# Performance work log

Measured on AMD Instinct MI355X. Metric: run time of the kernel, lower is better.

Reference implementation:

```python
import jax, jax.numpy as jnp
import numpy as np

B, T, D, N = 32, 512, 128, 1024
NOISE = 0.001
SPECTRAL_RADIUS = 1.0


def setup_inputs() -> dict:
    key = jax.random.key(0)
    ks = jax.random.split(key, 7)
    x = jax.random.normal(ks[0], (B, T, D), dtype=jnp.float32)
    # w_input = uniform[0,1)*2 - 1
    w_input = jax.random.uniform(ks[1], (D, N), dtype=jnp.float32) * 2 - 1
    # w_reservoir = uniform[0,1) - 0.5, then rescaled to target spectral radius
    w_res = jax.random.uniform(ks[2], (N, N), dtype=jnp.float32) - 0.5
    radius = float(np.max(np.abs(np.linalg.eigvals(np.asarray(w_res, dtype=np.float32)))))
    w_res = w_res * jnp.float32(SPECTRAL_RADIUS / radius)
    w_scale_input = jax.random.uniform(ks[3], (), dtype=jnp.float32)
    states0 = jax.random.normal(ks[4], (B, N), dtype=jnp.float32)
    step0 = jax.random.normal(ks[5], (B, N), dtype=jnp.float32)
    random_noise = jax.random.normal(ks[6], (B, N), dtype=jnp.float32)
    return {
        "x": x,
        "w_input": w_input,
        "w_reservoir": w_res,
        "w_scale_input": w_scale_input,
        "states0": states0,
        "step0": step0,
        "random_noise": random_noise,
    }


def reference(x, w_input, w_reservoir, w_scale_input, states0, step0, random_noise):
    # Precompute scaled input projections for steps 1..T-1 (parallel matmul)
    xin = jnp.einsum("btd,dn->btn", x[:, 1:, :], w_input) * w_scale_input  # [B,T-1,N]

    def step(states, xt):
        pre = states @ w_reservoir + xt
        post = jnp.tanh(pre) + NOISE * random_noise
        return post, post

    _, ys = jax.lax.scan(step, states0, jnp.swapaxes(xin, 0, 1))  # ys: [T-1,B,N]
    out = jnp.concatenate([step0[:, None, :], jnp.swapaxes(ys, 0, 1)], axis=1)  # [B,T,N]
    return out[..., None]  # [B,T,N,1]
```

## Files before the change

### kernel.cpp

```cpp
#include <hip/hip_runtime.h>
#include <hip/hip_bf16.h>
#include <math.h>

#define B_  32
#define T_  512
#define D_  128
#define N_  1024
#define NOISE_ 0.001f

#define NBLK 64
#define CPB  16

typedef __attribute__((ext_vector_type(8))) short  bf16x8;
typedef __attribute__((ext_vector_type(4))) float  f32x4;

static __device__ __forceinline__ unsigned short f2bf_rn(float f) {
    unsigned int u = __builtin_bit_cast(unsigned int, f);
    unsigned int r = (u + 0x7FFFu + ((u >> 16) & 1u)) >> 16;
    return (unsigned short)r;
}
static __device__ __forceinline__ float bf2f(unsigned short h) {
    return __builtin_bit_cast(float, (unsigned int)h << 16);
}

__global__ __launch_bounds__(256) void xin_gemm(
    const float* __restrict__ x, const float* __restrict__ w_in,
    const float* __restrict__ scale_p, float* __restrict__ out) {
  __shared__ float As[64 * 132];
  __shared__ float Bs[128 * 68];
  const int tid = threadIdx.x;
  const int bm = blockIdx.x;
  const int bn = blockIdx.y;

  {
    const f32x4* xg = (const f32x4*)(x + (size_t)bm * 64 * 128);
#pragma unroll
    for (int i = 0; i < 8; ++i) {
      int idx = tid + i * 256;
      int r = idx >> 5, c4 = idx & 31;
      f32x4 v = xg[idx];
      float* dst = &As[r * 132 + c4 * 4];
      dst[0] = v.x; dst[1] = v.y; dst[2] = v.z; dst[3] = v.w;
    }
  }
  {
#pragma unroll
    for (int i = 0; i < 8; ++i) {
      int idx = tid + i * 256;
      int r = idx >> 4, c4 = idx & 15;
      f32x4 v = *(const f32x4*)(w_in + (size_t)r * N_ + bn * 64 + c4 * 4);
      float* dst = &Bs[r * 68 + c4 * 4];
      dst[0] = v.x; dst[1] = v.y; dst[2] = v.z; dst[3] = v.w;
    }
  }
  __syncthreads();

  const int tx = tid & 15, ty = tid >> 4;
  float acc[4][4] = {};
  for (int k = 0; k < 128; ++k) {
    float a0 = As[(ty * 4 + 0) * 132 + k];
    float a1 = As[(ty * 4 + 1) * 132 + k];
    float a2 = As[(ty * 4 + 2) * 132 + k];
    float a3 = As[(ty * 4 + 3) * 132 + k];
    f32x4 bv = *(const f32x4*)&Bs[k * 68 + tx * 4];
#pragma unroll
    for (int j = 0; j < 4; ++j) {
      acc[0][j] += a0 * bv[j];
      acc[1][j] += a1 * bv[j];
      acc[2][j] += a2 * bv[j];
      acc[3][j] += a3 * bv[j];
    }
  }
  const float s = scale_p[0];
#pragma unroll
  for (int i = 0; i < 4; ++i) {
    int row = bm * 64 + ty * 4 + i;
    if ((row & 511) == 0) continue;
    f32x4 o;
    o.x = acc[i][0] * s; o.y = acc[i][1] * s;
    o.z = acc[i][2] * s; o.w = acc[i][3] * s;
    *(f32x4*)(out + (size_t)row * N_ + bn * 64 + tx * 4) = o;
  }
}

__global__ __launch_bounds__(256) void init_k(
    const float* __restrict__ states0, const float* __restrict__ step0,
    float* __restrict__ out, unsigned short* __restrict__ st_hi,
    unsigned short* __restrict__ st_lo, int* __restrict__ flags) {
  int i = blockIdx.x * 256 + threadIdx.x;
  if (i < B_ * N_) {
    int b = i >> 10, n = i & 1023;
    out[((size_t)b * T_ + 0) * N_ + n] = step0[i];
    float sv = states0[i];
    unsigned short h = f2bf_rn(sv);
    st_hi[i] = h;
    st_lo[i] = f2bf_rn(sv - bf2f(h));
  }
  if (i < 1024) flags[i] = 0;
}

__global__ __launch_bounds__(256, 1) void esn_rec(
    const float* __restrict__ w_res, const float* __restrict__ rn,
    float* __restrict__ out, unsigned short* __restrict__ st_hi,
    unsigned short* __restrict__ st_lo, int* flags) {
  __shared__ bf16x8 wHi8[CPB * 129];
  __shared__ bf16x8 wLo8[CPB * 129];
  __shared__ float  pLDS[4 * 32 * 17];

  const int tid = threadIdx.x;
  const int blk = blockIdx.x;

  {
    unsigned short* wH = (unsigned short*)wHi8;
    unsigned short* wL = (unsigned short*)wLo8;
    for (int i = tid; i < CPB * 1024; i += 256) {
      int c = i & 15, k = i >> 4;
      float wv = w_res[(size_t)k * N_ + blk * CPB + c];
      unsigned short h = f2bf_rn(wv);
      wH[c * 1032 + k] = h;
      wL[c * 1032 + k] = f2bf_rn(wv - bf2f(h));
    }
  }
  __syncthreads();

  const int lane = tid & 63, wave = tid >> 6;
  const int quad = lane >> 4, lm = lane & 15;

  const int rm = tid >> 3;
  const int cp = (tid & 7) * 2;
  const int colg = blk * CPB + cp;
  float2 nz = *(const float2*)&rn[(size_t)rm * N_ + colg];
  nz.x *= NOISE_; nz.y *= NOISE_;

  const int vo0 = lm * 2048 + wave * 512 + quad * 16;
  const int vo1 = vo0 + 16 * 2048;

  for (int t = 1; t < T_; ++t) {
    const int pc = (t - 1) & 1, ncur = t & 1;

    size_t o0 = ((size_t)rm * T_ + t) * N_ + colg;
    float2 xv = *(const float2*)&out[o0];

    {
      const int need = t - 1;
      const int fidx = (wave * 16 + (lane & 15)) * 16;
      while (true) {
        int f = __hip_atomic_load(&flags[fidx], __ATOMIC_RELAXED,
                                  __HIP_MEMORY_SCOPE_SYSTEM);
        if (__all(f >= need)) break;
      }
    }

    const char* baseH = (const char*)(st_hi + pc * (B_ * N_));
    const char* baseL = (const char*)(st_lo + pc * (B_ * N_));
    bf16x8 AH0[8], AH1[8], AL0[8], AL1[8];
#pragma unroll
    for (int kk = 0; kk < 8; ++kk) {
      int oa = vo0 + kk * 64, ob = vo1 + kk * 64;
      asm volatile("global_load_dwordx4 %0, %1, %2 sc0 sc1"
                   : "=v"(AH0[kk]) : "v"(oa), "s"(baseH) : "memory");
      asm volatile("global_load_dwordx4 %0, %1, %2 sc0 sc1"
                   : "=v"(AH1[kk]) : "v"(ob), "s"(baseH) : "memory");
      asm volatile("global_load_dwordx4 %0, %1, %2 sc0 sc1"
                   : "=v"(AL0[kk]) : "v"(oa), "s"(baseL) : "memory");
      asm volatile("global_load_dwordx4 %0, %1, %2 sc0 sc1"
                   : "=v"(AL1[kk]) : "v"(ob), "s"(baseL) : "memory");
    }
    asm volatile("s_waitcnt vmcnt(0)" ::: "memory");

    f32x4 acc0 = {0.f, 0.f, 0.f, 0.f};
    f32x4 acc1 = {0.f, 0.f, 0.f, 0.f};
#pragma unroll
    for (int kk = 0; kk < 8; ++kk) {
      const int k8 = wave * 32 + kk * 4 + quad;
      bf16x8 bh = wHi8[lm * 129 + k8];
      bf16x8 bl = wLo8[lm * 129 + k8];
      acc0 = __builtin_amdgcn_mfma_f32_16x16x32_bf16(AH0[kk], bh, acc0, 0, 0, 0);
      acc1 = __builtin_amdgcn_mfma_f32_16x16x32_bf16(AH1[kk], bh, acc1, 0, 0, 0);
      acc0 = __builtin_amdgcn_mfma_f32_16x16x32_bf16(AL0[kk], bh, acc0, 0, 0, 0);
      acc1 = __builtin_amdgcn_mfma_f32_16x16x32_bf16(AL1[kk], bh, acc1, 0, 0, 0);
      acc0 = __builtin_amdgcn_mfma_f32_16x16x32_bf16(AH0[kk], bl, acc0, 0, 0, 0);
      acc1 = __builtin_amdgcn_mfma_f32_16x16x32_bf16(AH1[kk], bl, acc1, 0, 0, 0);
    }

#pragma unroll
    for (int r = 0; r < 4; ++r) {
      pLDS[wave * 544 + (quad * 4 + r) * 17 + lm]      = acc0[r];
      pLDS[wave * 544 + (quad * 4 + r + 16) * 17 + lm] = acc1[r];
    }
    __syncthreads();

    float sa = pLDS[0 * 544 + rm * 17 + cp] + pLDS[1 * 544 + rm * 17 + cp]
             + pLDS[2 * 544 + rm * 17 + cp] + pLDS[3 * 544 + rm * 17 + cp];
    float sb = pLDS[0 * 544 + rm * 17 + cp + 1] + pLDS[1 * 544 + rm * 17 + cp + 1]
             + pLDS[2 * 544 + rm * 17 + cp + 1] + pLDS[3 * 544 + rm * 17 + cp + 1];
    float v0 = tanhf(sa + xv.x) + nz.x;
    float v1 = tanhf(sb + xv.y) + nz.y;
    float2 ov; ov.x = v0; ov.y = v1;
    *(float2*)&out[o0] = ov;

    unsigned short h0 = f2bf_rn(v0), h1 = f2bf_rn(v1);
    unsigned short l0 = f2bf_rn(v0 - bf2f(h0)), l1 = f2bf_rn(v1 - bf2f(h1));
    unsigned int hpack = (unsigned int)h0 | ((unsigned int)h1 << 16);
    unsigned int lpack = (unsigned int)l0 | ((unsigned int)l1 << 16);
    unsigned int* dh = (unsigned int*)(st_hi + ncur * (B_ * N_) + (size_t)rm * N_ + colg);
    unsigned int* dl = (unsigned int*)(st_lo + ncur * (B_ * N_) + (size_t)rm * N_ + colg);
    __hip_atomic_store(dh, hpack, __ATOMIC_RELAXED, __HIP_MEMORY_SCOPE_SYSTEM);
    __hip_atomic_store(dl, lpack, __ATOMIC_RELAXED, __HIP_MEMORY_SCOPE_SYSTEM);

    asm volatile("s_waitcnt vmcnt(0)" ::: "memory");
    __syncthreads();
    if (tid == 0) {
      __hip_atomic_store(&flags[blk * 16], t, __ATOMIC_RELAXED,
                         __HIP_MEMORY_SCOPE_SYSTEM);
    }
  }
}

extern "C" void kernel_launch(void* const* d_in, const int* in_sizes, int n_in,
                              void* d_out, int out_size, void* d_ws, size_t ws_size,
                              hipStream_t stream) {
  const float* x       = (const float*)d_in[0];
  const float* w_in    = (const float*)d_in[1];
  const float* w_res   = (const float*)d_in[2];
  const float* wscale  = (const float*)d_in[3];
  const float* states0 = (const float*)d_in[4];
  const float* step0   = (const float*)d_in[5];
  const float* rnoise  = (const float*)d_in[6];
  float* out = (float*)d_out;

  char* ws = (char*)d_ws;
  unsigned short* st_hi = (unsigned short*)ws;
  unsigned short* st_lo = (unsigned short*)(ws + 131072);
  int* flags            = (int*)(ws + 262144);

  xin_gemm<<<dim3(256, 16), 256, 0, stream>>>(x, w_in, wscale, out);
  init_k<<<128, 256, 0, stream>>>(states0, step0, out, st_hi, st_lo, flags);
  esn_rec<<<NBLK, 256, 0, stream>>>(w_res, rnoise, out, st_hi, st_lo, flags);
}
```

Before: 3.118 ms.

## Hold reservoir weights in registers, halve workgroups, overlap state loads with MFMA

The persistent recurrence kernel now runs on 32 workgroups of 32 columns each instead of 64 of 16. The hi/lo bf16 weight slices live in VGPRs rather than LDS, which removes the per-step LDS weight reads. Each step issues its state loads and then starts MFMAs on the first half once those loads land, overlapping the rest of the load latency with compute. Fewer workgroups means fewer flags to poll per step, at the cost of more per-workgroup MFMA work and high register pressure.

```diff
diff --git a/kernel.cpp b/kernel.cpp
--- a/kernel.cpp
+++ b/kernel.cpp
@@ -8,8 +8,8 @@
 #define N_  1024
 #define NOISE_ 0.001f
 
-#define NBLK 64
-#define CPB  16
+#define NWORK 32
+#define CPB   32
 
 typedef __attribute__((ext_vector_type(8))) short  bf16x8;
 typedef __attribute__((ext_vector_type(4))) float  f32x4;
@@ -103,47 +103,60 @@
     const float* __restrict__ w_res, const float* __restrict__ rn,
     float* __restrict__ out, unsigned short* __restrict__ st_hi,
     unsigned short* __restrict__ st_lo, int* flags) {
-  __shared__ bf16x8 wHi8[CPB * 129];
-  __shared__ bf16x8 wLo8[CPB * 129];
-  __shared__ float  pLDS[4 * 32 * 17];
+  __shared__ float pLDS[4 * 32 * 33];
 
   const int tid = threadIdx.x;
   const int blk = blockIdx.x;
 
-  {
-    unsigned short* wH = (unsigned short*)wHi8;
-    unsigned short* wL = (unsigned short*)wLo8;
-    for (int i = tid; i < CPB * 1024; i += 256) {
-      int c = i & 15, k = i >> 4;
-      float wv = w_res[(size_t)k * N_ + blk * CPB + c];
-      unsigned short h = f2bf_rn(wv);
-      wH[c * 1032 + k] = h;
-      wL[c * 1032 + k] = f2bf_rn(wv - bf2f(h));
-    }
-  }
-  __syncthreads();
-
   const int lane = tid & 63, wave = tid >> 6;
   const int quad = lane >> 4, lm = lane & 15;
 
+  bf16x8 BH[8][2], BL[8][2];
+#pragma unroll
+  for (int kk = 0; kk < 8; ++kk) {
+#pragma unroll
+    for (int ct = 0; ct < 2; ++ct) {
+      const float* wp = w_res + (size_t)(wave * 256 + kk * 32 + quad * 8) * N_
+                              + blk * CPB + ct * 16 + lm;
+      bf16x8 hv, lv;
+#pragma unroll
+      for (int j = 0; j < 8; ++j) {
+        float wv = wp[(size_t)j * N_];
+        unsigned short h = f2bf_rn(wv);
+        hv[j] = (short)h;
+        lv[j] = (short)f2bf_rn(wv - bf2f(h));
+      }
+      BH[kk][ct] = hv;
+      BL[kk][ct] = lv;
+    }
+  }
+
   const int rm = tid >> 3;
-  const int cp = (tid & 7) * 2;
-  const int colg = blk * CPB + cp;
-  float2 nz = *(const float2*)&rn[(size_t)rm * N_ + colg];
-  nz.x *= NOISE_; nz.y *= NOISE_;
+  const int cg = (tid & 7) * 4;
+  const int colg = blk * CPB + cg;
+  float4 nz = *(const float4*)&rn[(size_t)rm * N_ + colg];
+  nz.x *= NOISE_; nz.y *= NOISE_; nz.z *= NOISE_; nz.w *= NOISE_;
 
   const int vo0 = lm * 2048 + wave * 512 + quad * 16;
   const int vo1 = vo0 + 16 * 2048;
+  const int fidx = (wave * 8 + (lane & 7)) * 16;
+
+  __syncthreads();
 
   for (int t = 1; t < T_; ++t) {
     const int pc = (t - 1) & 1, ncur = t & 1;
 
     size_t o0 = ((size_t)rm * T_ + t) * N_ + colg;
-    float2 xv = *(const float2*)&out[o0];
+    f32x4 xv;
+    {
+      int loff = (int)(o0 * 4);
+      const char* ob = (const char*)out;
+      asm volatile("global_load_dwordx4 %0, %1, %2"
+                   : "=v"(xv) : "v"(loff), "s"(ob) : "memory");
+    }
 
     {
       const int need = t - 1;
-      const int fidx = (wave * 16 + (lane & 15)) * 16;
       while (true) {
         int f = __hip_atomic_load(&flags[fidx], __ATOMIC_RELAXED,
                                   __HIP_MEMORY_SCOPE_SYSTEM);
@@ -166,47 +179,85 @@
       asm volatile("global_load_dwordx4 %0, %1, %2 sc0 sc1"
                    : "=v"(AL1[kk]) : "v"(ob), "s"(baseL) : "memory");
     }
+
+    f32x4 acc00 = {0.f, 0.f, 0.f, 0.f};
+    f32x4 acc01 = {0.f, 0.f, 0.f, 0.f};
+    f32x4 acc10 = {0.f, 0.f, 0.f, 0.f};
+    f32x4 acc11 = {0.f, 0.f, 0.f, 0.f};
+
+    asm volatile("s_waitcnt vmcnt(16)" ::: "memory");
+    __builtin_amdgcn_sched_barrier(0);
+#pragma unroll
+    for (int kk = 0; kk < 4; ++kk) {
+      acc00 = __builtin_amdgcn_mfma_f32_16x16x32_bf16(AH0[kk], BH[kk][0], acc00, 0, 0, 0);
+      acc01 = __builtin_amdgcn_mfma_f32_16x16x32_bf16(AH1[kk], BH[kk][0], acc01, 0, 0, 0);
+      acc10 = __builtin_amdgcn_mfma_f32_16x16x32_bf16(AH0[kk], BH[kk][1], acc10, 0, 0, 0);
+      acc11 = __builtin_amdgcn_mfma_f32_16x16x32_bf16(AH1[kk], BH[kk][1], acc11, 0, 0, 0);
+      acc00 = __builtin_amdgcn_mfma_f32_16x16x32_bf16(AL0[kk], BH[kk][0], acc00, 0, 0, 0);
+      acc01 = __builtin_amdgcn_mfma_f32_16x16x32_bf16(AL1[kk], BH[kk][0], acc01, 0, 0, 0);
+      acc10 = __builtin_amdgcn_mfma_f32_16x16x32_bf16(AL0[kk], BH[kk][1], acc10, 0, 0, 0);
+      acc11 = __builtin_amdgcn_mfma_f32_16x16x32_bf16(AL1[kk], BH[kk][1], acc11, 0, 0, 0);
+      acc00 = __builtin_amdgcn_mfma_f32_16x16x32_bf16(AH0[kk], BL[kk][0], acc00, 0, 0, 0);
+      acc01 = __builtin_amdgcn_mfma_f32_16x16x32_bf16(AH1[kk], BL[kk][0], acc01, 0, 0, 0);
+      acc10 = __builtin_amdgcn_mfma_f32_16x16x32_bf16(AH0[kk], BL[kk][1], acc10, 0, 0, 0);
+      acc11 = __builtin_amdgcn_mfma_f32_16x16x32_bf16(AH1[kk], BL[kk][1], acc11, 0, 0, 0);
+    }
     asm volatile("s_waitcnt vmcnt(0)" ::: "memory");
-
-    f32x4 acc0 = {0.f, 0.f, 0.f, 0.f};
-    f32x4 acc1 = {0.f, 0.f, 0.f, 0.f};
-#pragma unroll
-    for (int kk = 0; kk < 8; ++kk) {
-      const int k8 = wave * 32 + kk * 4 + quad;
-      bf16x8 bh = wHi8[lm * 129 + k8];
-      bf16x8 bl = wLo8[lm * 129 + k8];
-      acc0 = __builtin_amdgcn_mfma_f32_16x16x32_bf16(AH0[kk], bh, acc0, 0, 0, 0);
-      acc1 = __builtin_amdgcn_mfma_f32_16x16x32_bf16(AH1[kk], bh, acc1, 0, 0, 0);
-      acc0 = __builtin_amdgcn_mfma_f32_16x16x32_bf16(AL0[kk], bh, acc0, 0, 0, 0);
-      acc1 = __builtin_amdgcn_mfma_f32_16x16x32_bf16(AL1[kk], bh, acc1, 0, 0, 0);
-      acc0 = __builtin_amdgcn_mfma_f32_16x16x32_bf16(AH0[kk], bl, acc0, 0, 0, 0);
-      acc1 = __builtin_amdgcn_mfma_f32_16x16x32_bf16(AH1[kk], bl, acc1, 0, 0, 0);
+    __builtin_amdgcn_sched_barrier(0);
+#pragma unroll
+    for (int kk = 4; kk < 8; ++kk) {
+      acc00 = __builtin_amdgcn_mfma_f32_16x16x32_bf16(AH0[kk], BH[kk][0], acc00, 0, 0, 0);
+      acc01 = __builtin_amdgcn_mfma_f32_16x16x32_bf16(AH1[kk], BH[kk][0], acc01, 0, 0, 0);
+      acc10 = __builtin_amdgcn_mfma_f32_16x16x32_bf16(AH0[kk], BH[kk][1], acc10, 0, 0, 0);
+      acc11 = __builtin_amdgcn_mfma_f32_16x16x32_bf16(AH1[kk], BH[kk][1], acc11, 0, 0, 0);
+      acc00 = __builtin_amdgcn_mfma_f32_16x16x32_bf16(AL0[kk], BH[kk][0], acc00, 0, 0, 0);
+      acc01 = __builtin_amdgcn_mfma_f32_16x16x32_bf16(AL1[kk], BH[kk][0], acc01, 0, 0, 0);
+      acc10 = __builtin_amdgcn_mfma_f32_16x16x32_bf16(AL0[kk], BH[kk][1], acc10, 0, 0, 0);
+      acc11 = __builtin_amdgcn_mfma_f32_16x16x32_bf16(AL1[kk], BH[kk][1], acc11, 0, 0, 0);
+      acc00 = __builtin_amdgcn_mfma_f32_16x16x32_bf16(AH0[kk], BL[kk][0], acc00, 0, 0, 0);
+      acc01 = __builtin_amdgcn_mfma_f32_16x16x32_bf16(AH1[kk], BL[kk][0], acc01, 0, 0, 0);
+      acc10 = __builtin_amdgcn_mfma_f32_16x16x32_bf16(AH0[kk], BL[kk][1], acc10, 0, 0, 0);
+      acc11 = __builtin_amdgcn_mfma_f32_16x16x32_bf16(AH1[kk], BL[kk][1], acc11, 0, 0, 0);
     }
 
 #pragma unroll
     for (int r = 0; r < 4; ++r) {
-      pLDS[wave * 544 + (quad * 4 + r) * 17 + lm]      = acc0[r];
-      pLDS[wave * 544 + (quad * 4 + r + 16) * 17 + lm] = acc1[r];
+      pLDS[wave * 1056 + (quad * 4 + r) * 33 + lm]           = acc00[r];
+      pLDS[wave * 1056 + (quad * 4 + r + 16) * 33 + lm]      = acc01[r];
+      pLDS[wave * 1056 + (quad * 4 + r) * 33 + 16 + lm]      = acc10[r];
+      pLDS[wave * 1056 + (quad * 4 + r + 16) * 33 + 16 + lm] = acc11[r];
     }
     __syncthreads();
 
-    float sa = pLDS[0 * 544 + rm * 17 + cp] + pLDS[1 * 544 + rm * 17 + cp]
-             + pLDS[2 * 544 + rm * 17 + cp] + pLDS[3 * 544 + rm * 17 + cp];
-    float sb = pLDS[0 * 544 + rm * 17 + cp + 1] + pLDS[1 * 544 + rm * 17 + cp + 1]
-             + pLDS[2 * 544 + rm * 17 + cp + 1] + pLDS[3 * 544 + rm * 17 + cp + 1];
-    float v0 = tanhf(sa + xv.x) + nz.x;
-    float v1 = tanhf(sb + xv.y) + nz.y;
-    float2 ov; ov.x = v0; ov.y = v1;
-    *(float2*)&out[o0] = ov;
+    float s0 = 0.f, s1 = 0.f, s2 = 0.f, s3 = 0.f;
+#pragma unroll
+    for (int w = 0; w < 4; ++w) {
+      const float* p = &pLDS[w * 1056 + rm * 33 + cg];
+      s0 += p[0]; s1 += p[1]; s2 += p[2]; s3 += p[3];
+    }
+    float v0 = tanhf(s0 + xv[0]) + nz.x;
+    float v1 = tanhf(s1 + xv[1]) + nz.y;
+    float v2 = tanhf(s2 + xv[2]) + nz.z;
+    float v3 = tanhf(s3 + xv[3]) + nz.w;
+    float4 ov; ov.x = v0; ov.y = v1; ov.z = v2; ov.w = v3;
+    *(float4*)&out[o0] = ov;
 
     unsigned short h0 = f2bf_rn(v0), h1 = f2bf_rn(v1);
+    unsigned short h2 = f2bf_rn(v2), h3 = f2bf_rn(v3);
     unsigned short l0 = f2bf_rn(v0 - bf2f(h0)), l1 = f2bf_rn(v1 - bf2f(h1));
-    unsigned int hpack = (unsigned int)h0 | ((unsigned int)h1 << 16);
-    unsigned int lpack = (unsigned int)l0 | ((unsigned int)l1 << 16);
-    unsigned int* dh = (unsigned int*)(st_hi + ncur * (B_ * N_) + (size_t)rm * N_ + colg);
-    unsigned int* dl = (unsigned int*)(st_lo + ncur * (B_ * N_) + (size_t)rm * N_ + colg);
-    __hip_atomic_store(dh, hpack, __ATOMIC_RELAXED, __HIP_MEMORY_SCOPE_SYSTEM);
-    __hip_atomic_store(dl, lpack, __ATOMIC_RELAXED, __HIP_MEMORY_SCOPE_SYSTEM);
+    unsigned short l2 = f2bf_rn(v2 - bf2f(h2)), l3 = f2bf_rn(v3 - bf2f(h3));
+    unsigned long long hp =
+        (unsigned long long)((unsigned int)h0 | ((unsigned int)h1 << 16)) |
+        ((unsigned long long)((unsigned int)h2 | ((unsigned int)h3 << 16)) << 32);
+    unsigned long long lp =
+        (unsigned long long)((unsigned int)l0 | ((unsigned int)l1 << 16)) |
+        ((unsigned long long)((unsigned int)l2 | ((unsigned int)l3 << 16)) << 32);
+    unsigned long long* dh =
+        (unsigned long long*)(st_hi + ncur * (B_ * N_) + (size_t)rm * N_ + colg);
+    unsigned long long* dl =
+        (unsigned long long*)(st_lo + ncur * (B_ * N_) + (size_t)rm * N_ + colg);
+    __hip_atomic_store(dh, hp, __ATOMIC_RELAXED, __HIP_MEMORY_SCOPE_SYSTEM);
+    __hip_atomic_store(dl, lp, __ATOMIC_RELAXED, __HIP_MEMORY_SCOPE_SYSTEM);
 
     asm volatile("s_waitcnt vmcnt(0)" ::: "memory");
     __syncthreads();
@@ -236,5 +287,5 @@
 
   xin_gemm<<<dim3(256, 16), 256, 0, stream>>>(x, w_in, wscale, out);
   init_k<<<128, 256, 0, stream>>>(states0, step0, out, st_hi, st_lo, flags);
-  esn_rec<<<NBLK, 256, 0, stream>>>(w_res, rnoise, out, st_hi, st_lo, flags);
-}
+  esn_rec<<<NWORK, 256, 0, stream>>>(w_res, rnoise, out, st_hi, st_lo, flags);
+}
```

Result: slower. 3.352 ms (+7.5%).

## Hold recurrent weights in registers and use per-wave flags with pipelined polling

Applied to the files above, without the earlier changes.

The recurrence kernel now keeps its bf16 hi/lo slices of the reservoir weights in VGPRs instead of LDS, removing the per-step LDS weight reads. Each wave publishes its own progress flag, so the end-of-step block barrier goes away. Flag polling uses two overlapping vector loads, and the MFMA chain starts on the first half of the state loads while the second half is still in flight. It also launches 192 extra spinner blocks that run dummy FMAs and loads until the recurrence finishes, apparently to keep the GPU busy or its clocks up. That costs power and risks deadlock if the worker blocks are not all resident together.

```diff
diff --git a/kernel.cpp b/kernel.cpp
--- a/kernel.cpp
+++ b/kernel.cpp
@@ -8,11 +8,14 @@
 #define N_  1024
 #define NOISE_ 0.001f
 
-#define NBLK 64
-#define CPB  16
+#define NWORK 64
+#define CPB   16
+#define GRID_REC 256
 
 typedef __attribute__((ext_vector_type(8))) short  bf16x8;
 typedef __attribute__((ext_vector_type(4))) float  f32x4;
+typedef __attribute__((ext_vector_type(2))) float  f32x2;
+typedef __attribute__((ext_vector_type(4))) int    i32x4;
 
 static __device__ __forceinline__ unsigned short f2bf_rn(float f) {
     unsigned int u = __builtin_bit_cast(unsigned int, f);
@@ -22,6 +25,7 @@
 static __device__ __forceinline__ float bf2f(unsigned short h) {
     return __builtin_bit_cast(float, (unsigned int)h << 16);
 }
+static __device__ __forceinline__ int imin(int a, int b) { return a < b ? a : b; }
 
 __global__ __launch_bounds__(256) void xin_gemm(
     const float* __restrict__ x, const float* __restrict__ w_in,
@@ -103,28 +107,54 @@
     const float* __restrict__ w_res, const float* __restrict__ rn,
     float* __restrict__ out, unsigned short* __restrict__ st_hi,
     unsigned short* __restrict__ st_lo, int* flags) {
-  __shared__ bf16x8 wHi8[CPB * 129];
-  __shared__ bf16x8 wLo8[CPB * 129];
-  __shared__ float  pLDS[4 * 32 * 17];
+  __shared__ float pLDS[4 * 32 * 17];
 
   const int tid = threadIdx.x;
-  const int blk = blockIdx.x;
-
-  {
-    unsigned short* wH = (unsigned short*)wHi8;
-    unsigned short* wL = (unsigned short*)wLo8;
-    for (int i = tid; i < CPB * 1024; i += 256) {
-      int c = i & 15, k = i >> 4;
-      float wv = w_res[(size_t)k * N_ + blk * CPB + c];
-      unsigned short h = f2bf_rn(wv);
-      wH[c * 1032 + k] = h;
-      wL[c * 1032 + k] = f2bf_rn(wv - bf2f(h));
-    }
-  }
-  __syncthreads();
-
+  const int bx = blockIdx.x;
+
+  if (bx >= NWORK) {
+    float hx = (float)(tid + bx);
+    const char* wb = (const char*)w_res;
+    int it = 0;
+    while (true) {
+      i32x4 f;
+      asm volatile("global_load_dwordx4 %0, %1, %2 sc0 sc1\n\ts_waitcnt vmcnt(0)"
+                   : "=v"(f) : "v"(0), "s"(flags) : "memory");
+      if (imin(imin(f.x, f.y), imin(f.z, f.w)) >= T_ - 1) break;
+#pragma unroll 8
+      for (int u = 0; u < 1024; ++u)
+        hx = __builtin_fmaf(hx, 1.0000001f, 1.0e-7f);
+      f32x4 dummy;
+      int off = (it & 16383) * 256;
+      asm volatile("global_load_dwordx4 %0, %1, %2 sc0\n\ts_waitcnt vmcnt(0)"
+                   : "=v"(dummy) : "v"(off), "s"(wb) : "memory");
+      asm volatile("" :: "v"(dummy));
+      ++it;
+    }
+    asm volatile("" :: "v"(hx));
+    return;
+  }
+
+  const int blk = bx;
   const int lane = tid & 63, wave = tid >> 6;
   const int quad = lane >> 4, lm = lane & 15;
+
+  bf16x8 BH[8], BL[8];
+#pragma unroll
+  for (int kk = 0; kk < 8; ++kk) {
+    const float* wp = w_res + (size_t)(wave * 256 + kk * 32 + quad * 8) * N_
+                            + blk * CPB + lm;
+    bf16x8 hv, lv;
+#pragma unroll
+    for (int j = 0; j < 8; ++j) {
+      float wv = wp[(size_t)j * N_];
+      unsigned short h = f2bf_rn(wv);
+      hv[j] = (short)h;
+      lv[j] = (short)f2bf_rn(wv - bf2f(h));
+    }
+    BH[kk] = hv;
+    BL[kk] = lv;
+  }
 
   const int rm = tid >> 3;
   const int cp = (tid & 7) * 2;
@@ -134,21 +164,40 @@
 
   const int vo0 = lm * 2048 + wave * 512 + quad * 16;
   const int vo1 = vo0 + 16 * 2048;
+  const int fbyte = (wave * 16 + (lane & 15)) * 64;
 
   for (int t = 1; t < T_; ++t) {
     const int pc = (t - 1) & 1, ncur = t & 1;
 
     size_t o0 = ((size_t)rm * T_ + t) * N_ + colg;
-    float2 xv = *(const float2*)&out[o0];
+    f32x2 xv;
+    {
+      int loff = (int)(o0 * 4);
+      asm volatile("global_load_dwordx2 %0, %1, %2"
+                   : "=v"(xv) : "v"(loff), "s"((const char*)out) : "memory");
+    }
 
     {
       const int need = t - 1;
-      const int fidx = (wave * 16 + (lane & 15)) * 16;
+      i32x4 fA, fB;
+      asm volatile("global_load_dwordx4 %0, %1, %2 sc0 sc1"
+                   : "=v"(fA) : "v"(fbyte), "s"(flags) : "memory");
+      asm volatile("global_load_dwordx4 %0, %1, %2 sc0 sc1"
+                   : "=v"(fB) : "v"(fbyte), "s"(flags) : "memory");
       while (true) {
-        int f = __hip_atomic_load(&flags[fidx], __ATOMIC_RELAXED,
-                                  __HIP_MEMORY_SCOPE_SYSTEM);
-        if (__all(f >= need)) break;
+        asm volatile("s_waitcnt vmcnt(1)" ::: "memory");
+        __builtin_amdgcn_sched_barrier(0);
+        if (__all(imin(imin(fA.x, fA.y), imin(fA.z, fA.w)) >= need)) break;
+        asm volatile("global_load_dwordx4 %0, %1, %2 sc0 sc1"
+                     : "=v"(fA) : "v"(fbyte), "s"(flags) : "memory");
+        asm volatile("s_waitcnt vmcnt(1)" ::: "memory");
+        __builtin_amdgcn_sched_barrier(0);
+        if (__all(imin(imin(fB.x, fB.y), imin(fB.z, fB.w)) >= need)) break;
+        asm volatile("global_load_dwordx4 %0, %1, %2 sc0 sc1"
+                     : "=v"(fB) : "v"(fbyte), "s"(flags) : "memory");
       }
+      asm volatile("s_waitcnt vmcnt(0)" ::: "memory");
+      __builtin_amdgcn_sched_barrier(0);
     }
 
     const char* baseH = (const char*)(st_hi + pc * (B_ * N_));
@@ -166,21 +215,31 @@
       asm volatile("global_load_dwordx4 %0, %1, %2 sc0 sc1"
                    : "=v"(AL1[kk]) : "v"(ob), "s"(baseL) : "memory");
     }
-    asm volatile("s_waitcnt vmcnt(0)" ::: "memory");
 
     f32x4 acc0 = {0.f, 0.f, 0.f, 0.f};
     f32x4 acc1 = {0.f, 0.f, 0.f, 0.f};
-#pragma unroll
-    for (int kk = 0; kk < 8; ++kk) {
-      const int k8 = wave * 32 + kk * 4 + quad;
-      bf16x8 bh = wHi8[lm * 129 + k8];
-      bf16x8 bl = wLo8[lm * 129 + k8];
-      acc0 = __builtin_amdgcn_mfma_f32_16x16x32_bf16(AH0[kk], bh, acc0, 0, 0, 0);
-      acc1 = __builtin_amdgcn_mfma_f32_16x16x32_bf16(AH1[kk], bh, acc1, 0, 0, 0);
-      acc0 = __builtin_amdgcn_mfma_f32_16x16x32_bf16(AL0[kk], bh, acc0, 0, 0, 0);
-      acc1 = __builtin_amdgcn_mfma_f32_16x16x32_bf16(AL1[kk], bh, acc1, 0, 0, 0);
-      acc0 = __builtin_amdgcn_mfma_f32_16x16x32_bf16(AH0[kk], bl, acc0, 0, 0, 0);
-      acc1 = __builtin_amdgcn_mfma_f32_16x16x32_bf16(AH1[kk], bl, acc1, 0, 0, 0);
+
+    asm volatile("s_waitcnt vmcnt(16)" ::: "memory");
+    __builtin_amdgcn_sched_barrier(0);
+#pragma unroll
+    for (int kk = 0; kk < 4; ++kk) {
+      acc0 = __builtin_amdgcn_mfma_f32_16x16x32_bf16(AH0[kk], BH[kk], acc0, 0, 0, 0);
+      acc1 = __builtin_amdgcn_mfma_f32_16x16x32_bf16(AH1[kk], BH[kk], acc1, 0, 0, 0);
+      acc0 = __builtin_amdgcn_mfma_f32_16x16x32_bf16(AL0[kk], BH[kk], acc0, 0, 0, 0);
+      acc1 = __builtin_amdgcn_mfma_f32_16x16x32_bf16(AL1[kk], BH[kk], acc1, 0, 0, 0);
+      acc0 = __builtin_amdgcn_mfma_f32_16x16x32_bf16(AH0[kk], BL[kk], acc0, 0, 0, 0);
+      acc1 = __builtin_amdgcn_mfma_f32_16x16x32_bf16(AH1[kk], BL[kk], acc1, 0, 0, 0);
+    }
+    asm volatile("s_waitcnt vmcnt(0)" ::: "memory");
+    __builtin_amdgcn_sched_barrier(0);
+#pragma unroll
+    for (int kk = 4; kk < 8; ++kk) {
+      acc0 = __builtin_amdgcn_mfma_f32_16x16x32_bf16(AH0[kk], BH[kk], acc0, 0, 0, 0);
+      acc1 = __builtin_amdgcn_mfma_f32_16x16x32_bf16(AH1[kk], BH[kk], acc1, 0, 0, 0);
+      acc0 = __builtin_amdgcn_mfma_f32_16x16x32_bf16(AL0[kk], BH[kk], acc0, 0, 0, 0);
+      acc1 = __builtin_amdgcn_mfma_f32_16x16x32_bf16(AL1[kk], BH[kk], acc1, 0, 0, 0);
+      acc0 = __builtin_amdgcn_mfma_f32_16x16x32_bf16(AH0[kk], BL[kk], acc0, 0, 0, 0);
+      acc1 = __builtin_amdgcn_mfma_f32_16x16x32_bf16(AH1[kk], BL[kk], acc1, 0, 0, 0);
     }
 
 #pragma unroll
@@ -194,8 +253,10 @@
              + pLDS[2 * 544 + rm * 17 + cp] + pLDS[3 * 544 + rm * 17 + cp];
     float sb = pLDS[0 * 544 + rm * 17 + cp + 1] + pLDS[1 * 544 + rm * 17 + cp + 1]
              + pLDS[2 * 544 + rm * 17 + cp + 1] + pLDS[3 * 544 + rm * 17 + cp + 1];
-    float v0 = tanhf(sa + xv.x) + nz.x;
-    float v1 = tanhf(sb + xv.y) + nz.y;
+    __syncthreads();
+
+    float v0 = tanhf(sa + xv[0]) + nz.x;
+    float v1 = tanhf(sb + xv[1]) + nz.y;
     float2 ov; ov.x = v0; ov.y = v1;
     *(float2*)&out[o0] = ov;
 
@@ -209,10 +270,9 @@
     __hip_atomic_store(dl, lpack, __ATOMIC_RELAXED, __HIP_MEMORY_SCOPE_SYSTEM);
 
     asm volatile("s_waitcnt vmcnt(0)" ::: "memory");
-    __syncthreads();
-    if (tid == 0) {
-      __hip_atomic_store(&flags[blk * 16], t, __ATOMIC_RELAXED,
-                         __HIP_MEMORY_SCOPE_SYSTEM);
+    if (lane == 0) {
+      asm volatile("global_store_dword %0, %1, %2 sc0 sc1"
+                   :: "v"((blk * 16 + wave) * 4), "v"(t), "s"(flags) : "memory");
     }
   }
 }
@@ -236,5 +296,5 @@
 
   xin_gemm<<<dim3(256, 16), 256, 0, stream>>>(x, w_in, wscale, out);
   init_k<<<128, 256, 0, stream>>>(states0, step0, out, st_hi, st_lo, flags);
-  esn_rec<<<NBLK, 256, 0, stream>>>(w_res, rnoise, out, st_hi, st_lo, flags);
-}
+  esn_rec<<<GRID_REC, 256, 0, stream>>>(w_res, rnoise, out, st_hi, st_lo, flags);
+}
```

New measurement: 3.367 ms. 8.0% more time.

## Embed parity tags in packed state words to replace flag-based inter-block sync

Applied to the files above, without the earlier changes.

Replaces the per-block flag barrier with step-parity bits stored in the low bit of the bf16 low-part words. The hi/lo state is interleaved into 16-byte packets written by one store, and consumers spin on a sentinel word and then validate every loaded packet's tag before using it. This removes the store-wait-syncthreads-flag round trip on each step. It also moves the reservoir weight slices from LDS into registers. The cost is a lost LSB in the lo part, extra tag checks and possible reload loops, and higher register pressure.

```diff
diff --git a/kernel.cpp b/kernel.cpp
--- a/kernel.cpp
+++ b/kernel.cpp
@@ -8,11 +8,13 @@
 #define N_  1024
 #define NOISE_ 0.001f
 
-#define NBLK 64
-#define CPB  16
+#define NWORK 64
+#define CPB   16
+#define SLOT_BYTES 131072
 
 typedef __attribute__((ext_vector_type(8))) short  bf16x8;
 typedef __attribute__((ext_vector_type(4))) float  f32x4;
+typedef __attribute__((ext_vector_type(4))) int    i32x4;
 
 static __device__ __forceinline__ unsigned short f2bf_rn(float f) {
     unsigned int u = __builtin_bit_cast(unsigned int, f);
@@ -85,46 +87,61 @@
 
 __global__ __launch_bounds__(256) void init_k(
     const float* __restrict__ states0, const float* __restrict__ step0,
-    float* __restrict__ out, unsigned short* __restrict__ st_hi,
-    unsigned short* __restrict__ st_lo, int* __restrict__ flags) {
+    float* __restrict__ out, char* __restrict__ stp) {
   int i = blockIdx.x * 256 + threadIdx.x;
   if (i < B_ * N_) {
     int b = i >> 10, n = i & 1023;
     out[((size_t)b * T_ + 0) * N_ + n] = step0[i];
-    float sv = states0[i];
-    unsigned short h = f2bf_rn(sv);
-    st_hi[i] = h;
-    st_lo[i] = f2bf_rn(sv - bf2f(h));
-  }
-  if (i < 1024) flags[i] = 0;
+  }
+  if (i < B_ * N_ / 4) {
+    int r = i >> 8, g = i & 255;
+    const float* sp = states0 + (size_t)r * N_ + g * 4;
+    unsigned int hw[4], lw[4];
+#pragma unroll
+    for (int j = 0; j < 4; ++j) {
+      float sv = sp[j];
+      unsigned short h = f2bf_rn(sv);
+      unsigned short l = f2bf_rn(sv - bf2f(h));
+      hw[j] = h;
+      lw[j] = (unsigned int)(l & 0xFFFEu);
+    }
+    i32x4 pkt;
+    pkt.x = (int)(hw[0] | (hw[1] << 16));
+    pkt.y = (int)(lw[0] | (lw[1] << 16));
+    pkt.z = (int)(hw[2] | (hw[3] << 16));
+    pkt.w = (int)(lw[2] | (lw[3] << 16));
+    *(i32x4*)(stp + (size_t)i * 16) = pkt;
+    i32x4 f1; f1.x = 0; f1.y = 0x00010000; f1.z = 0; f1.w = 0x00010000;
+    *(i32x4*)(stp + SLOT_BYTES + (size_t)i * 16) = f1;
+  }
 }
 
 __global__ __launch_bounds__(256, 1) void esn_rec(
     const float* __restrict__ w_res, const float* __restrict__ rn,
-    float* __restrict__ out, unsigned short* __restrict__ st_hi,
-    unsigned short* __restrict__ st_lo, int* flags) {
-  __shared__ bf16x8 wHi8[CPB * 129];
-  __shared__ bf16x8 wLo8[CPB * 129];
-  __shared__ float  pLDS[4 * 32 * 17];
+    float* __restrict__ out, char* stp) {
+  __shared__ float pLDS[4 * 32 * 17];
 
   const int tid = threadIdx.x;
   const int blk = blockIdx.x;
-
-  {
-    unsigned short* wH = (unsigned short*)wHi8;
-    unsigned short* wL = (unsigned short*)wLo8;
-    for (int i = tid; i < CPB * 1024; i += 256) {
-      int c = i & 15, k = i >> 4;
-      float wv = w_res[(size_t)k * N_ + blk * CPB + c];
-      unsigned short h = f2bf_rn(wv);
-      wH[c * 1032 + k] = h;
-      wL[c * 1032 + k] = f2bf_rn(wv - bf2f(h));
-    }
-  }
-  __syncthreads();
-
   const int lane = tid & 63, wave = tid >> 6;
   const int quad = lane >> 4, lm = lane & 15;
+
+  bf16x8 BH[8], BL[8];
+#pragma unroll
+  for (int kk = 0; kk < 8; ++kk) {
+    const float* wp = w_res + (size_t)(wave * 256 + kk * 32 + quad * 8) * N_
+                            + blk * CPB + lm;
+    bf16x8 hv, lv;
+#pragma unroll
+    for (int j = 0; j < 8; ++j) {
+      float wv = wp[(size_t)j * N_];
+      unsigned short h = f2bf_rn(wv);
+      hv[j] = (short)h;
+      lv[j] = (short)f2bf_rn(wv - bf2f(h));
+    }
+    BH[kk] = hv;
+    BL[kk] = lv;
+  }
 
   const int rm = tid >> 3;
   const int cp = (tid & 7) * 2;
@@ -132,55 +149,74 @@
   float2 nz = *(const float2*)&rn[(size_t)rm * N_ + colg];
   nz.x *= NOISE_; nz.y *= NOISE_;
 
-  const int vo0 = lm * 2048 + wave * 512 + quad * 16;
-  const int vo1 = vo0 + 16 * 2048;
+  const int vo0 = lm * 4096 + wave * 1024 + quad * 32;
+  const int vo1 = vo0 + 16 * 4096;
+  const int pp = wave * 16 + (lane & 15);
+  const int pbyte = ((lane >> 4) * 8 + 7) * 4096 + (pp * 4 + (lane >> 4)) * 16 + 4;
+  const int so = rm * 4096 + (blk * 4 + (cp >> 2)) * 16;
 
   for (int t = 1; t < T_; ++t) {
-    const int pc = (t - 1) & 1, ncur = t & 1;
+    const char* slotR = stp + ((t - 1) & 1) * SLOT_BYTES;
+    char* slotW = stp + (t & 1) * SLOT_BYTES;
+    const int want = ((t - 1) & 1) | ((((t - 1) >> 1) & 1) << 16);
 
     size_t o0 = ((size_t)rm * T_ + t) * N_ + colg;
     float2 xv = *(const float2*)&out[o0];
 
     {
-      const int need = t - 1;
-      const int fidx = (wave * 16 + (lane & 15)) * 16;
-      while (true) {
-        int f = __hip_atomic_load(&flags[fidx], __ATOMIC_RELAXED,
-                                  __HIP_MEMORY_SCOPE_SYSTEM);
-        if (__all(f >= need)) break;
+      int pr;
+      do {
+        asm volatile("global_load_dword %0, %1, %2 sc0 sc1\n\ts_waitcnt vmcnt(0)"
+                     : "=v"(pr) : "v"(pbyte), "s"(slotR) : "memory");
+      } while (!__all((pr & 0x00010001) == want));
+    }
+
+    i32x4 PA[8], PB[8], PC[8], PD[8];
+    while (true) {
+#pragma unroll
+      for (int kk = 0; kk < 8; ++kk) {
+        int oa = vo0 + kk * 128, ob = vo1 + kk * 128;
+        asm volatile("global_load_dwordx4 %0, %1, %2 sc0 sc1"
+                     : "=v"(PA[kk]) : "v"(oa), "s"(slotR) : "memory");
+        asm volatile("global_load_dwordx4 %0, %1, %2 sc0 sc1"
+                     : "=v"(PB[kk]) : "v"(oa + 16), "s"(slotR) : "memory");
+        asm volatile("global_load_dwordx4 %0, %1, %2 sc0 sc1"
+                     : "=v"(PC[kk]) : "v"(ob), "s"(slotR) : "memory");
+        asm volatile("global_load_dwordx4 %0, %1, %2 sc0 sc1"
+                     : "=v"(PD[kk]) : "v"(ob + 16), "s"(slotR) : "memory");
       }
-    }
-
-    const char* baseH = (const char*)(st_hi + pc * (B_ * N_));
-    const char* baseL = (const char*)(st_lo + pc * (B_ * N_));
-    bf16x8 AH0[8], AH1[8], AL0[8], AL1[8];
-#pragma unroll
-    for (int kk = 0; kk < 8; ++kk) {
-      int oa = vo0 + kk * 64, ob = vo1 + kk * 64;
-      asm volatile("global_load_dwordx4 %0, %1, %2 sc0 sc1"
-                   : "=v"(AH0[kk]) : "v"(oa), "s"(baseH) : "memory");
-      asm volatile("global_load_dwordx4 %0, %1, %2 sc0 sc1"
-                   : "=v"(AH1[kk]) : "v"(ob), "s"(baseH) : "memory");
-      asm volatile("global_load_dwordx4 %0, %1, %2 sc0 sc1"
-                   : "=v"(AL0[kk]) : "v"(oa), "s"(baseL) : "memory");
-      asm volatile("global_load_dwordx4 %0, %1, %2 sc0 sc1"
-                   : "=v"(AL1[kk]) : "v"(ob), "s"(baseL) : "memory");
-    }
-    asm volatile("s_waitcnt vmcnt(0)" ::: "memory");
+      asm volatile("s_waitcnt vmcnt(0)" ::: "memory");
+      __builtin_amdgcn_sched_barrier(0);
+      int err = 0;
+#pragma unroll
+      for (int kk = 0; kk < 8; ++kk) {
+        err |= (PA[kk].y ^ want) | (PA[kk].w ^ want);
+        err |= (PB[kk].y ^ want) | (PB[kk].w ^ want);
+        err |= (PC[kk].y ^ want) | (PC[kk].w ^ want);
+        err |= (PD[kk].y ^ want) | (PD[kk].w ^ want);
+      }
+      if (__all((err & 0x00010001) == 0)) break;
+    }
 
     f32x4 acc0 = {0.f, 0.f, 0.f, 0.f};
     f32x4 acc1 = {0.f, 0.f, 0.f, 0.f};
 #pragma unroll
     for (int kk = 0; kk < 8; ++kk) {
-      const int k8 = wave * 32 + kk * 4 + quad;
-      bf16x8 bh = wHi8[lm * 129 + k8];
-      bf16x8 bl = wLo8[lm * 129 + k8];
-      acc0 = __builtin_amdgcn_mfma_f32_16x16x32_bf16(AH0[kk], bh, acc0, 0, 0, 0);
-      acc1 = __builtin_amdgcn_mfma_f32_16x16x32_bf16(AH1[kk], bh, acc1, 0, 0, 0);
-      acc0 = __builtin_amdgcn_mfma_f32_16x16x32_bf16(AL0[kk], bh, acc0, 0, 0, 0);
-      acc1 = __builtin_amdgcn_mfma_f32_16x16x32_bf16(AL1[kk], bh, acc1, 0, 0, 0);
-      acc0 = __builtin_amdgcn_mfma_f32_16x16x32_bf16(AH0[kk], bl, acc0, 0, 0, 0);
-      acc1 = __builtin_amdgcn_mfma_f32_16x16x32_bf16(AH1[kk], bl, acc1, 0, 0, 0);
+      i32x4 h0i, l0i, h1i, l1i;
+      h0i.x = PA[kk].x; h0i.y = PA[kk].z; h0i.z = PB[kk].x; h0i.w = PB[kk].z;
+      l0i.x = PA[kk].y; l0i.y = PA[kk].w; l0i.z = PB[kk].y; l0i.w = PB[kk].w;
+      h1i.x = PC[kk].x; h1i.y = PC[kk].z; h1i.z = PD[kk].x; h1i.w = PD[kk].z;
+      l1i.x = PC[kk].y; l1i.y = PC[kk].w; l1i.z = PD[kk].y; l1i.w = PD[kk].w;
+      bf16x8 AH0 = __builtin_bit_cast(bf16x8, h0i);
+      bf16x8 AL0 = __builtin_bit_cast(bf16x8, l0i);
+      bf16x8 AH1 = __builtin_bit_cast(bf16x8, h1i);
+      bf16x8 AL1 = __builtin_bit_cast(bf16x8, l1i);
+      acc0 = __builtin_amdgcn_mfma_f32_16x16x32_bf16(AH0, BH[kk], acc0, 0, 0, 0);
+      acc1 = __builtin_amdgcn_mfma_f32_16x16x32_bf16(AH1, BH[kk], acc1, 0, 0, 0);
+      acc0 = __builtin_amdgcn_mfma_f32_16x16x32_bf16(AL0, BH[kk], acc0, 0, 0, 0);
+      acc1 = __builtin_amdgcn_mfma_f32_16x16x32_bf16(AL1, BH[kk], acc1, 0, 0, 0);
+      acc0 = __builtin_amdgcn_mfma_f32_16x16x32_bf16(AH0, BL[kk], acc0, 0, 0, 0);
+      acc1 = __builtin_amdgcn_mfma_f32_16x16x32_bf16(AH1, BL[kk], acc1, 0, 0, 0);
     }
 
 #pragma unroll
@@ -194,25 +230,30 @@
              + pLDS[2 * 544 + rm * 17 + cp] + pLDS[3 * 544 + rm * 17 + cp];
     float sb = pLDS[0 * 544 + rm * 17 + cp + 1] + pLDS[1 * 544 + rm * 17 + cp + 1]
              + pLDS[2 * 544 + rm * 17 + cp + 1] + pLDS[3 * 544 + rm * 17 + cp + 1];
+    __syncthreads();
+
     float v0 = tanhf(sa + xv.x) + nz.x;
     float v1 = tanhf(sb + xv.y) + nz.y;
     float2 ov; ov.x = v0; ov.y = v1;
     *(float2*)&out[o0] = ov;
 
-    unsigned short h0 = f2bf_rn(v0), h1 = f2bf_rn(v1);
-    unsigned short l0 = f2bf_rn(v0 - bf2f(h0)), l1 = f2bf_rn(v1 - bf2f(h1));
-    unsigned int hpack = (unsigned int)h0 | ((unsigned int)h1 << 16);
-    unsigned int lpack = (unsigned int)l0 | ((unsigned int)l1 << 16);
-    unsigned int* dh = (unsigned int*)(st_hi + ncur * (B_ * N_) + (size_t)rm * N_ + colg);
-    unsigned int* dl = (unsigned int*)(st_lo + ncur * (B_ * N_) + (size_t)rm * N_ + colg);
-    __hip_atomic_store(dh, hpack, __ATOMIC_RELAXED, __HIP_MEMORY_SCOPE_SYSTEM);
-    __hip_atomic_store(dl, lpack, __ATOMIC_RELAXED, __HIP_MEMORY_SCOPE_SYSTEM);
-
-    asm volatile("s_waitcnt vmcnt(0)" ::: "memory");
-    __syncthreads();
-    if (tid == 0) {
-      __hip_atomic_store(&flags[blk * 16], t, __ATOMIC_RELAXED,
-                         __HIP_MEMORY_SCOPE_SYSTEM);
+    float pv0 = __shfl_xor(v0, 1);
+    float pv1 = __shfl_xor(v1, 1);
+    if ((tid & 1) == 0) {
+      unsigned int b0 = (unsigned int)(t & 1), b1 = (unsigned int)((t >> 1) & 1);
+      unsigned short h0 = f2bf_rn(v0),  h1 = f2bf_rn(v1);
+      unsigned short h2 = f2bf_rn(pv0), h3 = f2bf_rn(pv1);
+      unsigned int l0 = ((unsigned int)f2bf_rn(v0  - bf2f(h0)) & 0xFFFEu) | b0;
+      unsigned int l1 = ((unsigned int)f2bf_rn(v1  - bf2f(h1)) & 0xFFFEu) | b1;
+      unsigned int l2 = ((unsigned int)f2bf_rn(pv0 - bf2f(h2)) & 0xFFFEu) | b0;
+      unsigned int l3 = ((unsigned int)f2bf_rn(pv1 - bf2f(h3)) & 0xFFFEu) | b1;
+      i32x4 pkt;
+      pkt.x = (int)((unsigned int)h0 | ((unsigned int)h1 << 16));
+      pkt.y = (int)(l0 | (l1 << 16));
+      pkt.z = (int)((unsigned int)h2 | ((unsigned int)h3 << 16));
+      pkt.w = (int)(l2 | (l3 << 16));
+      asm volatile("global_store_dwordx4 %0, %1, %2 sc0 sc1"
+                   :: "v"(so), "v"(pkt), "s"(slotW) : "memory");
     }
   }
 }
@@ -229,12 +270,9 @@
   const float* rnoise  = (const float*)d_in[6];
   float* out = (float*)d_out;
 
-  char* ws = (char*)d_ws;
-  unsigned short* st_hi = (unsigned short*)ws;
-  unsigned short* st_lo = (unsigned short*)(ws + 131072);
-  int* flags            = (int*)(ws + 262144);
+  char* stp = (char*)d_ws;
 
   xin_gemm<<<dim3(256, 16), 256, 0, stream>>>(x, w_in, wscale, out);
-  init_k<<<128, 256, 0, stream>>>(states0, step0, out, st_hi, st_lo, flags);
-  esn_rec<<<NBLK, 256, 0, stream>>>(w_res, rnoise, out, st_hi, st_lo, flags);
-}
+  init_k<<<128, 256, 0, stream>>>(states0, step0, out, stp);
+  esn_rec<<<NWORK, 256, 0, stream>>>(w_res, rnoise, out, stp);
+}
```

Result: slower. 3.205 ms (+2.8%).
